# Kernel tuning notes

Measured on AMD Instinct MI355X. Metric: run time of the kernel, lower is better.

The kernel has to match this reference:

```python
import jax, jax.numpy as jnp
import numpy as np

V, E, F, L, S, B, C = 30522, 768, 3072, 4, 512, 32, 2


def _layernorm(x, g, b, eps=1e-5):
    mu = jnp.mean(x, axis=-1, keepdims=True)
    var = jnp.var(x, axis=-1, keepdims=True)
    return (x - mu) * jax.lax.rsqrt(var + eps) * g + b


def setup_inputs() -> dict:
    key = jax.random.key(0)
    ks = jax.random.split(key, 24)
    s = 0.02
    inp = {
        "input_ids": jax.random.randint(ks[0], (S, B), 0, V),
        "tok_emb": jax.random.normal(ks[1], (V, E), jnp.float32) * s,
        "pos_emb": jax.random.normal(ks[2], (512, E), jnp.float32) * s,
        "Wq": jax.random.normal(ks[3], (L, E, E), jnp.float32) * s,
        "bq": jnp.zeros((L, E), jnp.float32),
        "Wk": jax.random.normal(ks[4], (L, E, E), jnp.float32) * s,
        "bk": jnp.zeros((L, E), jnp.float32),
        "Wv": jax.random.normal(ks[5], (L, E, E), jnp.float32) * s,
        "bv": jnp.zeros((L, E), jnp.float32),
        "Wo": jax.random.normal(ks[6], (L, E, E), jnp.float32) * s,
        "bo": jnp.zeros((L, E), jnp.float32),
        "g1": jnp.ones((L, E), jnp.float32),
        "beta1": jnp.zeros((L, E), jnp.float32),
        "g2": jnp.ones((L, E), jnp.float32),
        "beta2": jnp.zeros((L, E), jnp.float32),
        "W1": jax.random.normal(ks[7], (L, E, F), jnp.float32) * s,
        "bf1": jnp.zeros((L, F), jnp.float32),
        "W2": jax.random.normal(ks[8], (L, F, E), jnp.float32) * s,
        "bf2": jnp.zeros((L, E), jnp.float32),
        "Wc": jax.random.normal(ks[9], (E, C), jnp.float32) * s,
        "bc": jnp.zeros((C,), jnp.float32),
    }
    return inp


def reference(input_ids, tok_emb, pos_emb, Wq, bq, Wk, bk, Wv, bv, Wo, bo,
              g1, beta1, g2, beta2, W1, bf1, W2, bf2, Wc, bc):
    s_len = input_ids.shape[0]
    # x: [S, B, E] (seq-first, as in the original)
    x = tok_emb[input_ids] + pos_emb[jnp.arange(s_len)][:, None, :]
    scale = 1.0 / jnp.sqrt(jnp.asarray(E, x.dtype))
    for l in range(L):
        Q = x @ Wq[l] + bq[l]
        K = x @ Wk[l] + bk[l]
        Vv = x @ Wv[l] + bv[l]
        # NOTE: faithful to source bug: attention mixes over BATCH dim, scores [S,B,B]
        scores = jnp.einsum('sbe,sce->sbc', Q, K) * scale
        attn = jax.nn.softmax(scores, axis=-1)
        ao = jnp.einsum('sbc,sce->sbe', attn, Vv)
        ao = ao @ Wo[l] + bo[l]
        x = _layernorm(x + ao, g1[l], beta1[l])
        h = jax.nn.relu(x @ W1[l] + bf1[l]) @ W2[l] + bf2[l]
        x = _layernorm(x + h, g2[l], beta2[l])
    cls = x[0]                      # [B, E]
    return cls @ Wc + bc            # [B, C]
```

## Files before the change

kernel.cpp:

```cpp
#include <hip/hip_runtime.h>


#define E_DIM 768
#define F_DIM 3072
#define L_NUM 4
#define S_LEN 512
#define NTOK  (S_LEN * 32)
#define QKVN  (3 * E_DIM)

typedef float f32x4 __attribute__((ext_vector_type(4)));
typedef unsigned int u32x4 __attribute__((ext_vector_type(4)));
typedef unsigned short u16x4 __attribute__((ext_vector_type(4)));

__device__ __forceinline__ float bf2f(unsigned int bits) {
    return __uint_as_float(bits << 16);
}
__device__ __forceinline__ unsigned short f2bf(float f) {
    unsigned int x = __float_as_uint(f);
    return (unsigned short)((x + 0x7fffu + ((x >> 16) & 1u)) >> 16);
}

#define GLD16(gp, lp) \
    __builtin_amdgcn_global_load_lds( \
        (const __attribute__((address_space(1))) unsigned int*)(gp), \
        (__attribute__((address_space(3))) unsigned int*)(lp), 16, 0, 0)

__global__ __launch_bounds__(256)
void tr_k(const float* __restrict__ src, unsigned short* __restrict__ dst,
          int R, int C, size_t ss, size_t ds)
{
    __shared__ float tile[32][33];
    src += (size_t)blockIdx.z * ss;
    dst += (size_t)blockIdx.z * ds;
    const int r0 = blockIdx.y * 32, c0 = blockIdx.x * 32;
    const int tr = threadIdx.x >> 3, tc = (threadIdx.x & 7) * 4;
    f32x4 v = *(const f32x4*)(src + (size_t)(r0 + tr) * C + c0 + tc);
    tile[tr][tc + 0] = v[0]; tile[tr][tc + 1] = v[1];
    tile[tr][tc + 2] = v[2]; tile[tr][tc + 3] = v[3];
    __syncthreads();
    u16x4 o;
    o[0] = f2bf(tile[tc + 0][tr]); o[1] = f2bf(tile[tc + 1][tr]);
    o[2] = f2bf(tile[tc + 2][tr]); o[3] = f2bf(tile[tc + 3][tr]);
    *(u16x4*)(dst + (size_t)(c0 + tr) * R + r0 + tc) = o;
}

__global__ __launch_bounds__(256)
void biascat_k(const float* __restrict__ bq, const float* __restrict__ bk,
               const float* __restrict__ bv, float* __restrict__ bqkv)
{
    const int i = blockIdx.x * 256 + threadIdx.x;
    if (i >= L_NUM * QKVN) return;
    const int l = i / QKVN, n = i % QKVN;
    float v;
    if (n < 768)       v = bq[l * 768 + n];
    else if (n < 1536) v = bk[l * 768 + n - 768];
    else               v = bv[l * 768 + n - 1536];
    bqkv[i] = v;
}

__global__ __launch_bounds__(256)
void embed_k(const int* __restrict__ ids, const float* __restrict__ tok,
             const float* __restrict__ pos, float* __restrict__ xf,
             unsigned short* __restrict__ xb)
{
    const int row = blockIdx.x;
    const int s = row >> 5;
    const int id = ids[row];
    const size_t rb = (size_t)row * E_DIM;
    for (int e = threadIdx.x; e < E_DIM; e += 256) {
        float v = tok[(size_t)id * E_DIM + e] + pos[(size_t)s * E_DIM + e];
        xf[rb + e] = v;
        xb[rb + e] = f2bf(v);
    }
}

template<int MODE>
__global__ __launch_bounds__(256)
void gemm2_k(const unsigned short* __restrict__ A, const unsigned short* __restrict__ BT,
             const float* __restrict__ bias, void* __restrict__ Cout,
             int lda, int ldb, int ldc, int K, int JT)
{
    __shared__ unsigned short As[128 * 64];
    __shared__ unsigned short Bs[128 * 64];
    const int t = threadIdx.x;
    const int d = blockIdx.x;
    const int qd = d >> 3, rd = d & 7;
    const int jb = qd % JT;
    const int ib = rd + 8 * (qd / JT);
    const int i0 = ib * 128, j0 = jb * 128;

    const int lane = t & 63, wave = t >> 6;
    const int wm = wave >> 1, wn = wave & 1;
    const int lr = lane & 15, lg = lane >> 4;

    const int sr = t >> 3;
    const int sc = (t & 7) * 8;

    f32x4 acc[4][4];
    #pragma unroll
    for (int mf = 0; mf < 4; mf++)
        #pragma unroll
        for (int nf = 0; nf < 4; nf++) acc[mf][nf] = (f32x4)0.0f;

    const unsigned short* Ab = A  + (size_t)(i0 + sr) * lda + sc;
    const unsigned short* Bb = BT + (size_t)(j0 + sr) * ldb + sc;
    unsigned short* Asp = &As[sr * 64 + sc];
    unsigned short* Bsp = &Bs[sr * 64 + sc];

    for (int k0 = 0; k0 < K; k0 += 64) {
        __syncthreads();
        #pragma unroll
        for (int c = 0; c < 4; c++) {
            GLD16(Ab + (size_t)(32 * c) * lda + k0, Asp + 32 * c * 64);
            GLD16(Bb + (size_t)(32 * c) * ldb + k0, Bsp + 32 * c * 64);
        }
        asm volatile("s_waitcnt vmcnt(0)" ::: "memory");
        __syncthreads();
        #pragma unroll
        for (int kk = 0; kk < 64; kk += 32) {
            u32x4 a[4], b[4];
            #pragma unroll
            for (int f = 0; f < 4; f++) {
                a[f] = *(const u32x4*)(&As[(wm * 64 + f * 16 + lr) * 64 + kk + lg * 8]);
                b[f] = *(const u32x4*)(&Bs[(wn * 64 + f * 16 + lr) * 64 + kk + lg * 8]);
            }
            #pragma unroll
            for (int mf = 0; mf < 4; mf++)
                #pragma unroll
                for (int nf = 0; nf < 4; nf++)
                    asm volatile("v_mfma_f32_16x16x32_bf16 %0, %1, %2, %0"
                                 : "+v"(acc[mf][nf]) : "v"(a[mf]), "v"(b[nf]));
        }
    }
    asm volatile("s_nop 7\n\ts_nop 7");
    #pragma unroll
    for (int nf = 0; nf < 4; nf++) {
        const int col = j0 + wn * 64 + nf * 16 + lr;
        const float bv = bias ? bias[col] : 0.0f;
        #pragma unroll
        for (int mf = 0; mf < 4; mf++) {
            #pragma unroll
            for (int jj = 0; jj < 4; jj++) {
                const int row = i0 + wm * 64 + mf * 16 + lg * 4 + jj;
                const size_t idx = (size_t)row * ldc + col;
                float v = acc[mf][nf][jj] + bv;
                if (MODE == 1) v = fmaxf(v, 0.0f);
                if (MODE == 2) ((float*)Cout)[idx] += v;
                else           ((unsigned short*)Cout)[idx] = f2bf(v);
            }
        }
    }
}

__global__ __launch_bounds__(768)
void attn_k(unsigned short* __restrict__ qkv)
{
    __shared__ float attn_t[32 * 36];
    const int s = blockIdx.x;
    const int t = threadIdx.x;
    const int base = s * 32;

    if (t < 64) {
        const int lr = t & 15, lg = t >> 4;
        f32x4 sacc[2][2];
        #pragma unroll
        for (int m = 0; m < 2; m++)
            #pragma unroll
            for (int n = 0; n < 2; n++) sacc[m][n] = (f32x4)0.0f;
        const unsigned short* Qb = qkv + (size_t)base * QKVN;
        #pragma unroll 4
        for (int k0 = 0; k0 < E_DIM; k0 += 32) {
            u32x4 a0 = *(const u32x4*)(Qb + (size_t)lr        * QKVN + k0 + lg * 8);
            u32x4 a1 = *(const u32x4*)(Qb + (size_t)(16 + lr) * QKVN + k0 + lg * 8);
            u32x4 b0 = *(const u32x4*)(Qb + (size_t)lr        * QKVN + 768 + k0 + lg * 8);
            u32x4 b1 = *(const u32x4*)(Qb + (size_t)(16 + lr) * QKVN + 768 + k0 + lg * 8);
            asm volatile("v_mfma_f32_16x16x32_bf16 %0, %1, %2, %0" : "+v"(sacc[0][0]) : "v"(a0), "v"(b0));
            asm volatile("v_mfma_f32_16x16x32_bf16 %0, %1, %2, %0" : "+v"(sacc[0][1]) : "v"(a0), "v"(b1));
            asm volatile("v_mfma_f32_16x16x32_bf16 %0, %1, %2, %0" : "+v"(sacc[1][0]) : "v"(a1), "v"(b0));
            asm volatile("v_mfma_f32_16x16x32_bf16 %0, %1, %2, %0" : "+v"(sacc[1][1]) : "v"(a1), "v"(b1));
        }
        asm volatile("s_nop 7\n\ts_nop 7");
        const float scale = 0.036084391824351615f;
        float p[2][2][4];
        #pragma unroll
        for (int m = 0; m < 2; m++) {
            #pragma unroll
            for (int j = 0; j < 4; j++) {
                float v0 = sacc[m][0][j] * scale;
                float v1 = sacc[m][1][j] * scale;
                float mx = fmaxf(v0, v1);
                #pragma unroll
                for (int o = 1; o < 16; o <<= 1) mx = fmaxf(mx, __shfl_xor(mx, o));
                float e0 = expf(v0 - mx), e1 = expf(v1 - mx);
                float sm = e0 + e1;
                #pragma unroll
                for (int o = 1; o < 16; o <<= 1) sm += __shfl_xor(sm, o);
                const float r = 1.0f / sm;
                p[m][0][j] = e0 * r;
                p[m][1][j] = e1 * r;
            }
        }
        #pragma unroll
        for (int m = 0; m < 2; m++)
            #pragma unroll
            for (int n = 0; n < 2; n++)
                #pragma unroll
                for (int j = 0; j < 4; j++)
                    attn_t[(n * 16 + lr) * 36 + m * 16 + lg * 4 + j] = p[m][n][j];
    }
    __syncthreads();
    if (t < E_DIM) {
        float o[32];
        #pragma unroll
        for (int q = 0; q < 32; q++) o[q] = 0.f;
        for (int c = 0; c < 32; c++) {
            const float vv = bf2f(qkv[(size_t)(base + c) * QKVN + 1536 + t]);
            const f32x4* arow = (const f32x4*)(&attn_t[c * 36]);
            #pragma unroll
            for (int q8 = 0; q8 < 8; q8++) {
                f32x4 a4 = arow[q8];
                o[q8 * 4 + 0] += a4[0] * vv;
                o[q8 * 4 + 1] += a4[1] * vv;
                o[q8 * 4 + 2] += a4[2] * vv;
                o[q8 * 4 + 3] += a4[3] * vv;
            }
        }
        #pragma unroll
        for (int q = 0; q < 32; q++)
            qkv[(size_t)(base + q) * QKVN + t] = f2bf(o[q]);
    }
}

__global__ __launch_bounds__(256)
void ln_k(float* x, const float* __restrict__ g, const float* __restrict__ bta,
          unsigned short* __restrict__ xbo)
{
    __shared__ float red[8];
    const int row = blockIdx.x, t = threadIdx.x;
    const size_t rb = (size_t)row * E_DIM;
    float v[3];
    float s = 0.f, s2 = 0.f;
    #pragma unroll
    for (int i = 0; i < 3; i++) {
        const float a = x[rb + t + i * 256];
        v[i] = a; s += a; s2 += a * a;
    }
    #pragma unroll
    for (int o = 32; o > 0; o >>= 1) { s += __shfl_down(s, o); s2 += __shfl_down(s2, o); }
    const int wv_ = t >> 6;
    if ((t & 63) == 0) { red[wv_] = s; red[4 + wv_] = s2; }
    __syncthreads();
    if (t == 0) {
        red[0] = red[0] + red[1] + red[2] + red[3];
        red[4] = red[4] + red[5] + red[6] + red[7];
    }
    __syncthreads();
    const float mu   = red[0] * (1.f / E_DIM);
    const float var  = red[4] * (1.f / E_DIM) - mu * mu;
    const float rinv = rsqrtf(var + 1e-5f);
    #pragma unroll
    for (int i = 0; i < 3; i++) {
        const int e = t + i * 256;
        const float y = (v[i] - mu) * rinv * g[e] + bta[e];
        x[rb + e] = y;
        xbo[rb + e] = f2bf(y);
    }
}

__global__ __launch_bounds__(256)
void cls_k(const float* __restrict__ xf, const float* __restrict__ Wc,
           const float* __restrict__ bc, float* __restrict__ out)
{
    __shared__ float red[256];
    const int t = threadIdx.x;
    const int o = t >> 2, p = t & 3;
    const int b = o >> 1, c = o & 1;
    float acc = 0.f;
    for (int e = p; e < E_DIM; e += 4)
        acc += xf[(size_t)b * E_DIM + e] * Wc[e * 2 + c];
    red[t] = acc;
    __syncthreads();
    if (p == 0) out[o] = red[t] + red[t + 1] + red[t + 2] + red[t + 3] + bc[c];
}

extern "C" void kernel_launch(void* const* d_in, const int* in_sizes, int n_in,
                              void* d_out, int out_size, void* d_ws, size_t ws_size,
                              hipStream_t stream)
{
    (void)in_sizes; (void)n_in; (void)out_size;
    const int*   ids = (const int*)  d_in[0];
    const float* tok = (const float*)d_in[1];
    const float* pos = (const float*)d_in[2];
    const float* Wq  = (const float*)d_in[3];
    const float* bq  = (const float*)d_in[4];
    const float* Wk  = (const float*)d_in[5];
    const float* bk  = (const float*)d_in[6];
    const float* Wv  = (const float*)d_in[7];
    const float* bv  = (const float*)d_in[8];
    const float* Wo  = (const float*)d_in[9];
    const float* bo  = (const float*)d_in[10];
    const float* g1  = (const float*)d_in[11];
    const float* be1 = (const float*)d_in[12];
    const float* g2  = (const float*)d_in[13];
    const float* be2 = (const float*)d_in[14];
    const float* W1  = (const float*)d_in[15];
    const float* bf1 = (const float*)d_in[16];
    const float* W2  = (const float*)d_in[17];
    const float* bf2 = (const float*)d_in[18];
    const float* Wc  = (const float*)d_in[19];
    const float* bc  = (const float*)d_in[20];
    float* out = (float*)d_out;

    auto al = [](size_t b) { return (b + 255) & ~(size_t)255; };
    const size_t NE = (size_t)NTOK * E_DIM;
    const size_t sEE = (size_t)E_DIM * E_DIM, sEF = (size_t)E_DIM * F_DIM;
    const size_t fixed = al(NE * 4) + al(NE * 2)
                       + al((size_t)L_NUM * QKVN * E_DIM * 2) + al((size_t)L_NUM * sEE * 2)
                       + al((size_t)L_NUM * sEF * 2) + al((size_t)L_NUM * sEF * 2)
                       + al((size_t)L_NUM * QKVN * 4);
    const bool big = ws_size >= fixed + al((size_t)NTOK * F_DIM * 2);

    char* p = (char*)d_ws;
    auto carve = [&](size_t bytes) { char* r = p; p += (bytes + 255) & ~(size_t)255; return r; };
    float*          xf    = (float*)carve(NE * 4);
    unsigned short* xb    = (unsigned short*)carve(NE * 2);
    unsigned short* qkv   = (unsigned short*)carve(big ? (size_t)NTOK * F_DIM * 2
                                                       : (size_t)NTOK * QKVN * 2);
    unsigned short* wqkvT = (unsigned short*)carve((size_t)L_NUM * QKVN * E_DIM * 2);
    unsigned short* woT   = (unsigned short*)carve((size_t)L_NUM * sEE * 2);
    unsigned short* w1T   = (unsigned short*)carve((size_t)L_NUM * sEF * 2);
    unsigned short* w2T   = (unsigned short*)carve((size_t)L_NUM * sEF * 2);
    float*          bqkv  = (float*)carve((size_t)L_NUM * QKVN * 4);
    unsigned short* h1c   = qkv;

    tr_k<<<dim3(24, 24, 4), 256, 0, stream>>>(Wq, wqkvT,              768, 768, sEE, (size_t)QKVN * E_DIM);
    tr_k<<<dim3(24, 24, 4), 256, 0, stream>>>(Wk, wqkvT + 768 * 768,  768, 768, sEE, (size_t)QKVN * E_DIM);
    tr_k<<<dim3(24, 24, 4), 256, 0, stream>>>(Wv, wqkvT + 1536 * 768, 768, 768, sEE, (size_t)QKVN * E_DIM);
    tr_k<<<dim3(24, 24, 4), 256, 0, stream>>>(Wo, woT, 768, 768, sEE, sEE);
    tr_k<<<dim3(96, 24, 4), 256, 0, stream>>>(W1, w1T, 768, 3072, sEF, sEF);
    tr_k<<<dim3(24, 96, 4), 256, 0, stream>>>(W2, w2T, 3072, 768, sEF, sEF);
    biascat_k<<<(L_NUM * QKVN + 255) / 256, 256, 0, stream>>>(bq, bk, bv, bqkv);

    embed_k<<<NTOK, 256, 0, stream>>>(ids, tok, pos, xf, xb);

    const int IT = NTOK / 128;
    for (int l = 0; l < L_NUM; l++) {
        const unsigned short* wqkv_l = wqkvT + (size_t)l * QKVN * E_DIM;
        const unsigned short* wo_l   = woT + (size_t)l * sEE;
        const unsigned short* w1_l   = w1T + (size_t)l * sEF;
        const unsigned short* w2_l   = w2T + (size_t)l * sEF;

        gemm2_k<0><<<IT * 18, 256, 0, stream>>>(xb, wqkv_l, bqkv + l * QKVN, qkv,
                                                E_DIM, E_DIM, QKVN, E_DIM, 18);
        attn_k<<<S_LEN, 768, 0, stream>>>(qkv);
        gemm2_k<2><<<IT * 6, 256, 0, stream>>>(qkv, wo_l, bo + l * E_DIM, xf,
                                               QKVN, E_DIM, E_DIM, E_DIM, 6);
        ln_k<<<NTOK, 256, 0, stream>>>(xf, g1 + l * E_DIM, be1 + l * E_DIM, xb);
        if (big) {
            gemm2_k<1><<<IT * 24, 256, 0, stream>>>(xb, w1_l, bf1 + (size_t)l * F_DIM, h1c,
                                                    E_DIM, E_DIM, F_DIM, E_DIM, 24);
            gemm2_k<2><<<IT * 6, 256, 0, stream>>>(h1c, w2_l, bf2 + l * E_DIM, xf,
                                                   F_DIM, F_DIM, E_DIM, F_DIM, 6);
        } else {
            for (int c = 0; c < 2; c++) {
                const int c0 = c * 1536;
                gemm2_k<1><<<IT * 12, 256, 0, stream>>>(xb, w1_l + (size_t)c0 * E_DIM,
                                                        bf1 + (size_t)l * F_DIM + c0, h1c,
                                                        E_DIM, E_DIM, 1536, E_DIM, 12);
                gemm2_k<2><<<IT * 6, 256, 0, stream>>>(h1c, w2_l + c0,
                                                       c == 0 ? (bf2 + l * E_DIM) : (const float*)nullptr,
                                                       xf, 1536, F_DIM, E_DIM, 1536, 6);
            }
        }
        ln_k<<<NTOK, 256, 0, stream>>>(xf, g2 + l * E_DIM, be2 + l * E_DIM, xb);
    }

    cls_k<<<1, 256, 0, stream>>>(xf, Wc, bc, out);
}
```

Before: 1.870 ms.

## Replace GEMM with 256x256 double-buffered swizzled-LDS kernel using 8 waves

The bf16 MFMA GEMM moves from 128x128 tiles with 4 waves to 256x256 tiles with 8 waves. Global-to-LDS loads are double-buffered so the next K-slab streams in while MFMAs run. LDS chunks are XOR-swizzled to avoid bank conflicts, and s_setprio raises wave priority around the MFMA bursts. The goal is more data reuse per tile and hidden load latency. The cost is 128 KB of LDS per block and fewer blocks, which can leave CUs idle for the small N=768 GEMMs (192 blocks).

```diff
diff --git a/kernel.cpp b/kernel.cpp
--- a/kernel.cpp
+++ b/kernel.cpp
@@ -75,73 +75,101 @@
 }
 
 template<int MODE>
-__global__ __launch_bounds__(256)
-void gemm2_k(const unsigned short* __restrict__ A, const unsigned short* __restrict__ BT,
+__global__ __launch_bounds__(512, 2)
+void gemm3_k(const unsigned short* __restrict__ A, const unsigned short* __restrict__ BT,
              const float* __restrict__ bias, void* __restrict__ Cout,
              int lda, int ldb, int ldc, int K, int JT)
 {
-    __shared__ unsigned short As[128 * 64];
-    __shared__ unsigned short Bs[128 * 64];
+    __shared__ unsigned short As[2 * 256 * 64];
+    __shared__ unsigned short Bs[2 * 256 * 64];
     const int t = threadIdx.x;
     const int d = blockIdx.x;
     const int qd = d >> 3, rd = d & 7;
     const int jb = qd % JT;
     const int ib = rd + 8 * (qd / JT);
-    const int i0 = ib * 128, j0 = jb * 128;
+    const int i0 = ib * 256, j0 = jb * 256;
 
     const int lane = t & 63, wave = t >> 6;
-    const int wm = wave >> 1, wn = wave & 1;
+    const int wm = wave >> 2, wn = wave & 3;
     const int lr = lane & 15, lg = lane >> 4;
 
-    const int sr = t >> 3;
-    const int sc = (t & 7) * 8;
-
-    f32x4 acc[4][4];
+    const int strow = t >> 3;
+    const int stchk = (t & 7) ^ (strow & 7);
+    const unsigned short* Ab = A  + (size_t)(i0 + strow) * lda + stchk * 8;
+    const unsigned short* Bb = BT + (size_t)(j0 + strow) * ldb + stchk * 8;
+    const int ldst = t * 8;
+
+    f32x4 acc[8][4];
     #pragma unroll
-    for (int mf = 0; mf < 4; mf++)
+    for (int mf = 0; mf < 8; mf++)
         #pragma unroll
         for (int nf = 0; nf < 4; nf++) acc[mf][nf] = (f32x4)0.0f;
 
-    const unsigned short* Ab = A  + (size_t)(i0 + sr) * lda + sc;
-    const unsigned short* Bb = BT + (size_t)(j0 + sr) * ldb + sc;
-    unsigned short* Asp = &As[sr * 64 + sc];
-    unsigned short* Bsp = &Bs[sr * 64 + sc];
-
-    for (int k0 = 0; k0 < K; k0 += 64) {
-        __syncthreads();
-        #pragma unroll
-        for (int c = 0; c < 4; c++) {
-            GLD16(Ab + (size_t)(32 * c) * lda + k0, Asp + 32 * c * 64);
-            GLD16(Bb + (size_t)(32 * c) * ldb + k0, Bsp + 32 * c * 64);
-        }
-        asm volatile("s_waitcnt vmcnt(0)" ::: "memory");
-        __syncthreads();
-        #pragma unroll
-        for (int kk = 0; kk < 64; kk += 32) {
-            u32x4 a[4], b[4];
-            #pragma unroll
-            for (int f = 0; f < 4; f++) {
-                a[f] = *(const u32x4*)(&As[(wm * 64 + f * 16 + lr) * 64 + kk + lg * 8]);
-                b[f] = *(const u32x4*)(&Bs[(wn * 64 + f * 16 + lr) * 64 + kk + lg * 8]);
-            }
-            #pragma unroll
-            for (int mf = 0; mf < 4; mf++)
-                #pragma unroll
-                for (int nf = 0; nf < 4; nf++)
-                    asm volatile("v_mfma_f32_16x16x32_bf16 %0, %1, %2, %0"
-                                 : "+v"(acc[mf][nf]) : "v"(a[mf]), "v"(b[nf]));
-        }
-    }
+    const int rsw = (lg ^ (lr & 7)) * 8;
+    const int NT = K >> 6;
+
+#define STAGE3(k0, cbuf) do { \
+    _Pragma("unroll") \
+    for (int ii = 0; ii < 4; ii++) \
+        GLD16(Ab + (size_t)(ii * 64) * lda + (k0), &As[(cbuf) * 16384 + ii * 4096 + ldst]); \
+    _Pragma("unroll") \
+    for (int ii = 0; ii < 4; ii++) \
+        GLD16(Bb + (size_t)(ii * 64) * ldb + (k0), &Bs[(cbuf) * 16384 + ii * 4096 + ldst]); \
+} while (0)
+
+#define COMPUTE3(cbuf) do { \
+    _Pragma("unroll") \
+    for (int ks = 0; ks < 2; ks++) { \
+        u32x4 a[8], b[4]; \
+        _Pragma("unroll") \
+        for (int mf = 0; mf < 8; mf++) \
+            a[mf] = *(const u32x4*)(&As[(cbuf) * 16384 + (wm * 128 + mf * 16 + lr) * 64 + (rsw ^ (ks * 32))]); \
+        _Pragma("unroll") \
+        for (int nf = 0; nf < 4; nf++) \
+            b[nf] = *(const u32x4*)(&Bs[(cbuf) * 16384 + (wn * 64 + nf * 16 + lr) * 64 + (rsw ^ (ks * 32))]); \
+        __builtin_amdgcn_s_setprio(1); \
+        _Pragma("unroll") \
+        for (int mf = 0; mf < 8; mf++) \
+            _Pragma("unroll") \
+            for (int nf = 0; nf < 4; nf++) \
+                asm volatile("v_mfma_f32_16x16x32_bf16 %0, %1, %2, %0" \
+                             : "+v"(acc[mf][nf]) : "v"(a[mf]), "v"(b[nf])); \
+        __builtin_amdgcn_s_setprio(0); \
+    } \
+} while (0)
+
+    STAGE3(0, 0);
+    STAGE3(64, 1);
+
+    for (int kt = 0; kt < NT - 1; ++kt) {
+        asm volatile("s_waitcnt vmcnt(8)" ::: "memory");
+        __builtin_amdgcn_s_barrier();
+        asm volatile("" ::: "memory");
+        __builtin_amdgcn_sched_barrier(0);
+        COMPUTE3(kt & 1);
+        __builtin_amdgcn_sched_barrier(0);
+        asm volatile("" ::: "memory");
+        __builtin_amdgcn_s_barrier();
+        asm volatile("" ::: "memory");
+        if (kt + 2 < NT) STAGE3((kt + 2) * 64, kt & 1);
+        __builtin_amdgcn_sched_barrier(0);
+    }
+    asm volatile("s_waitcnt vmcnt(0)" ::: "memory");
+    __builtin_amdgcn_s_barrier();
+    asm volatile("" ::: "memory");
+    __builtin_amdgcn_sched_barrier(0);
+    COMPUTE3((NT - 1) & 1);
+
     asm volatile("s_nop 7\n\ts_nop 7");
     #pragma unroll
     for (int nf = 0; nf < 4; nf++) {
         const int col = j0 + wn * 64 + nf * 16 + lr;
         const float bv = bias ? bias[col] : 0.0f;
         #pragma unroll
-        for (int mf = 0; mf < 4; mf++) {
+        for (int mf = 0; mf < 8; mf++) {
             #pragma unroll
             for (int jj = 0; jj < 4; jj++) {
-                const int row = i0 + wm * 64 + mf * 16 + lg * 4 + jj;
+                const int row = i0 + wm * 128 + mf * 16 + lg * 4 + jj;
                 const size_t idx = (size_t)row * ldc + col;
                 float v = acc[mf][nf][jj] + bv;
                 if (MODE == 1) v = fmaxf(v, 0.0f);
@@ -150,6 +178,8 @@
             }
         }
     }
+#undef STAGE3
+#undef COMPUTE3
 }
 
 __global__ __launch_bounds__(768)
@@ -343,33 +373,32 @@
 
     embed_k<<<NTOK, 256, 0, stream>>>(ids, tok, pos, xf, xb);
 
-    const int IT = NTOK / 128;
     for (int l = 0; l < L_NUM; l++) {
         const unsigned short* wqkv_l = wqkvT + (size_t)l * QKVN * E_DIM;
         const unsigned short* wo_l   = woT + (size_t)l * sEE;
         const unsigned short* w1_l   = w1T + (size_t)l * sEF;
         const unsigned short* w2_l   = w2T + (size_t)l * sEF;
 
-        gemm2_k<0><<<IT * 18, 256, 0, stream>>>(xb, wqkv_l, bqkv + l * QKVN, qkv,
-                                                E_DIM, E_DIM, QKVN, E_DIM, 18);
+        gemm3_k<0><<<64 * 9, 512, 0, stream>>>(xb, wqkv_l, bqkv + l * QKVN, qkv,
+                                               E_DIM, E_DIM, QKVN, E_DIM, 9);
         attn_k<<<S_LEN, 768, 0, stream>>>(qkv);
-        gemm2_k<2><<<IT * 6, 256, 0, stream>>>(qkv, wo_l, bo + l * E_DIM, xf,
-                                               QKVN, E_DIM, E_DIM, E_DIM, 6);
+        gemm3_k<2><<<64 * 3, 512, 0, stream>>>(qkv, wo_l, bo + l * E_DIM, xf,
+                                               QKVN, E_DIM, E_DIM, E_DIM, 3);
         ln_k<<<NTOK, 256, 0, stream>>>(xf, g1 + l * E_DIM, be1 + l * E_DIM, xb);
         if (big) {
-            gemm2_k<1><<<IT * 24, 256, 0, stream>>>(xb, w1_l, bf1 + (size_t)l * F_DIM, h1c,
-                                                    E_DIM, E_DIM, F_DIM, E_DIM, 24);
-            gemm2_k<2><<<IT * 6, 256, 0, stream>>>(h1c, w2_l, bf2 + l * E_DIM, xf,
-                                                   F_DIM, F_DIM, E_DIM, F_DIM, 6);
+            gemm3_k<1><<<64 * 12, 512, 0, stream>>>(xb, w1_l, bf1 + (size_t)l * F_DIM, h1c,
+                                                    E_DIM, E_DIM, F_DIM, E_DIM, 12);
+            gemm3_k<2><<<64 * 3, 512, 0, stream>>>(h1c, w2_l, bf2 + l * E_DIM, xf,
+                                                   F_DIM, F_DIM, E_DIM, F_DIM, 3);
         } else {
             for (int c = 0; c < 2; c++) {
                 const int c0 = c * 1536;
-                gemm2_k<1><<<IT * 12, 256, 0, stream>>>(xb, w1_l + (size_t)c0 * E_DIM,
-                                                        bf1 + (size_t)l * F_DIM + c0, h1c,
-                                                        E_DIM, E_DIM, 1536, E_DIM, 12);
-                gemm2_k<2><<<IT * 6, 256, 0, stream>>>(h1c, w2_l + c0,
+                gemm3_k<1><<<64 * 6, 512, 0, stream>>>(xb, w1_l + (size_t)c0 * E_DIM,
+                                                       bf1 + (size_t)l * F_DIM + c0, h1c,
+                                                       E_DIM, E_DIM, 1536, E_DIM, 6);
+                gemm3_k<2><<<64 * 3, 512, 0, stream>>>(h1c, w2_l + c0,
                                                        c == 0 ? (bf2 + l * E_DIM) : (const float*)nullptr,
-                                                       xf, 1536, F_DIM, E_DIM, 1536, 6);
+                                                       xf, 1536, F_DIM, E_DIM, 1536, 3);
             }
         }
         ln_k<<<NTOK, 256, 0, stream>>>(xf, g2 + l * E_DIM, be2 + l * E_DIM, xb);
```

Measured after the change: 2.129 ms. +13.9%, slower.
